# Kernel tuning notes

Measured on AMD Instinct MI355X. Metric: run time of the kernel, lower is better.

The kernel has to match this reference:

```python
import jax, jax.numpy as jnp
import numpy as np

N = 50000      # nodes
E = 800000     # edges (before self-loops)
F_IN = 256
H = 8          # heads layer 1
C = 64         # hidden channels per head
OUT = 40       # classes
NEG_SLOPE = 0.2


def setup_inputs() -> dict:
    key = jax.random.key(0)
    ks = jax.random.split(key, 10)
    sc = 0.05
    return {
        "x": jax.random.normal(ks[0], (N, F_IN), jnp.float32),
        "edge_index": jax.random.randint(ks[1], (2, E), 0, N, dtype=jnp.int64),
        "W1": jax.random.normal(ks[2], (F_IN, H * C), jnp.float32) * sc,
        "a_src1": jax.random.normal(ks[3], (H, C), jnp.float32) * sc,
        "a_dst1": jax.random.normal(ks[4], (H, C), jnp.float32) * sc,
        "b1": jnp.zeros((H * C,), jnp.float32),
        "W2": jax.random.normal(ks[5], (H * C, OUT), jnp.float32) * sc,
        "a_src2": jax.random.normal(ks[6], (1, OUT), jnp.float32) * sc,
        "a_dst2": jax.random.normal(ks[7], (1, OUT), jnp.float32) * sc,
        "b2": jnp.zeros((OUT,), jnp.float32),
    }


def gat_layer(h_in, src, dst, W, a_s, a_d, b, heads, ch, concat, n):
    # h: [n, heads, ch] per-head linear transform
    h = (h_in @ W).reshape(n, heads, ch)
    alpha_s = jnp.sum(h * a_s, axis=-1)   # [n, heads]
    alpha_d = jnp.sum(h * a_d, axis=-1)   # [n, heads]
    # edge-wise raw attention logits [E, heads]
    e = jax.nn.leaky_relu(alpha_s[src] + alpha_d[dst], NEG_SLOPE)
    # segment softmax over incoming edges of each dst node
    m = jax.ops.segment_max(e, dst, num_segments=n)
    w = jnp.exp(e - m[dst])
    s = jax.ops.segment_sum(w, dst, num_segments=n)
    alpha = w / s[dst]                    # [E, heads]
    # scatter-aggregate messages: [n, heads, ch]
    out = jax.ops.segment_sum(h[src] * alpha[:, :, None], dst, num_segments=n)
    out = out.reshape(n, heads * ch) if concat else out.mean(axis=1)
    return out + b


def reference(x, edge_index, W1, a_src1, a_dst1, b1, W2, a_src2, a_dst2, b2):
    # add self-loops (PyG GATConv default); guarantees every dst has >=1 edge
    loop = jnp.arange(N, dtype=edge_index.dtype)
    src = jnp.concatenate([edge_index[0], loop])
    dst = jnp.concatenate([edge_index[1], loop])
    h = gat_layer(x, src, dst, W1, a_src1, a_dst1, b1, H, C, True, N)
    h = jax.nn.relu(h)  # dropout is identity in eval mode
    out = gat_layer(h, src, dst, W2, a_src2, a_dst2, b2, 1, OUT, False, N)
    return jax.nn.log_softmax(out, axis=1)
```

## Files before the change

### kernel.cpp

```cpp
#include <hip/hip_runtime.h>

#define N_NODES 50000
#define N_EDGES 800000
#define F_INK   256
#define HC      512
#define OUT_C   40
#define OUT_P   48
#define NEG     0.2f
#define CAP     64
#define GEMM_NB 782
#define CHUNKS  782
#define PART_SZ 6250
#define SCAT_NB (CHUNKS * 8)

typedef short short8 __attribute__((ext_vector_type(8)));
typedef float f32x4 __attribute__((ext_vector_type(4)));
typedef float f32x2 __attribute__((ext_vector_type(2)));

__device__ __forceinline__ float bf2f(unsigned short u) {
    union { unsigned int i; float f; } v; v.i = ((unsigned int)u) << 16; return v.f;
}
__device__ __forceinline__ unsigned short f2bf(float f) {
    union { float f; unsigned int i; } v; v.f = f;
    unsigned int x = v.i;
    return (unsigned short)((x + 0x7fffu + ((x >> 16) & 1u)) >> 16);
}
__device__ __forceinline__ float bflo(unsigned int u) {
    union { unsigned int i; float f; } v; v.i = u << 16; return v.f;
}
__device__ __forceinline__ float bfhi(unsigned int u) {
    union { unsigned int i; float f; } v; v.i = u & 0xffff0000u; return v.f;
}
__device__ __forceinline__ bool ei_is64(const int* ei) {
    return ei[1] == 0 && ei[3] == 0 && ei[5] == 0;
}
__device__ __forceinline__ float lrelu(float x) { return fmaxf(x, NEG * x); }
__device__ __forceinline__ unsigned char f2fp8(float v) {
    return (unsigned char)(__builtin_amdgcn_cvt_pk_fp8_f32(v, v, 0, false) & 0xff);
}
__device__ __forceinline__ float fp82f(unsigned char b) {
    f32x2 p = __builtin_amdgcn_cvt_pk_f32_fp8((int)b, false);
    return p[0];
}

__global__ __launch_bounds__(256) void prep_k(const float* __restrict__ W1, const float* __restrict__ W2,
                       const float* __restrict__ s1, const float* __restrict__ d1, const float* __restrict__ b1,
                       const float* __restrict__ s2, const float* __restrict__ d2, const float* __restrict__ b2,
                       unsigned short* __restrict__ W1p, unsigned short* __restrict__ W2p,
                       unsigned short* __restrict__ s1c, unsigned short* __restrict__ d1c,
                       unsigned short* __restrict__ b1c, unsigned short* __restrict__ s2c,
                       unsigned short* __restrict__ d2c, unsigned short* __restrict__ b2c,
                       int* __restrict__ cnt) {
    int b = blockIdx.x;
    if (b < 512) {
        int t = b * 256 + threadIdx.x;
        int k = t / HC, n = t % HC;
        int s = k >> 5, q = (k >> 3) & 3, j = k & 7;
        W1p[((((s << 2) + q) * HC + n) << 3) + j] = f2bf(W1[k * HC + n]);
    } else if (b < 608) {
        int t = (b - 512) * 256 + threadIdx.x;
        int k = t / OUT_P, n = t % OUT_P;
        int s = k >> 5, q = (k >> 3) & 3, j = k & 7;
        unsigned short v = (n < OUT_C) ? f2bf(W2[k * OUT_C + n]) : (unsigned short)0;
        W2p[((((s << 2) + q) * OUT_P + n) << 3) + j] = v;
    } else if (b == 608) {
        int t = threadIdx.x;
        for (int j = t; j < 512; j += 256) {
            s1c[j] = f2bf(s1[j]); d1c[j] = f2bf(d1[j]); b1c[j] = f2bf(b1[j]);
        }
        if (t < OUT_C) { s2c[t] = f2bf(s2[t]); d2c[t] = f2bf(d2[t]); b2c[t] = f2bf(b2[t]); }
    } else {
        int i = (b - 609) * 256 + threadIdx.x;
        if (i < N_NODES) cnt[i * 16] = 0;
    }
}

__global__ __launch_bounds__(256) void scat_k(const int* __restrict__ ei,
                                              int* __restrict__ cnt, int* __restrict__ srcs) {
    int tid = threadIdx.x;
    int part = blockIdx.x & 7;
    int chunk = blockIdx.x >> 3;
    int lo = part * PART_SZ;
    bool is64 = ei_is64(ei);
    int e0 = chunk * 1024 + (tid << 2);
    int s[4], d[4];
    bool vld[4];
    if (chunk < CHUNKS - 1) {
        if (is64) {
            int4 a0 = *reinterpret_cast<const int4*>(ei + 2 * e0);
            int4 a1 = *reinterpret_cast<const int4*>(ei + 2 * e0 + 4);
            int4 c0 = *reinterpret_cast<const int4*>(ei + 2 * N_EDGES + 2 * e0);
            int4 c1 = *reinterpret_cast<const int4*>(ei + 2 * N_EDGES + 2 * e0 + 4);
            s[0] = a0.x; s[1] = a0.z; s[2] = a1.x; s[3] = a1.z;
            d[0] = c0.x; d[1] = c0.z; d[2] = c1.x; d[3] = c1.z;
        } else {
            int4 a0 = *reinterpret_cast<const int4*>(ei + e0);
            int4 c0 = *reinterpret_cast<const int4*>(ei + N_EDGES + e0);
            s[0] = a0.x; s[1] = a0.y; s[2] = a0.z; s[3] = a0.w;
            d[0] = c0.x; d[1] = c0.y; d[2] = c0.z; d[3] = c0.w;
        }
        vld[0] = vld[1] = vld[2] = vld[3] = true;
    } else {
#pragma unroll
        for (int j = 0; j < 4; j++) {
            int e = e0 + j;
            vld[j] = e < N_EDGES;
            int ec = vld[j] ? e : 0;
            s[j] = is64 ? ei[2 * ec] : ei[ec];
            d[j] = is64 ? ei[2 * N_EDGES + 2 * ec] : ei[N_EDGES + ec];
        }
    }
#pragma unroll
    for (int j = 0; j < 4; j++) {
        int dj = d[j];
        if (vld[j] && dj >= lo && dj < lo + PART_SZ) {
            int pos = atomicAdd(&cnt[dj * 16], 1);
            if (pos < CAP) srcs[(size_t)dj * CAP + pos] = s[j];
        }
    }
}

__global__ __launch_bounds__(256) void gemm1_k(const float* __restrict__ x,
                                               const unsigned short* __restrict__ Wp,
                                               const unsigned short* __restrict__ a_s,
                                               const unsigned short* __restrict__ a_d,
                                               unsigned char* __restrict__ h1f8,
                                               float* __restrict__ as1, float* __restrict__ ad1) {
    __shared__ unsigned short xs[64 * 264];
    int tid = threadIdx.x;
    int bm = blockIdx.x;
    int row0 = bm * 64;
#pragma unroll
    for (int it = 0; it < 16; it++) {
        int j = tid + it * 256;
        int r = j >> 6;
        int c = (j & 63) << 2;
        int rr = row0 + r; rr = rr < N_NODES ? rr : N_NODES - 1;
        float4 f = *reinterpret_cast<const float4*>(x + (size_t)rr * F_INK + c);
        unsigned int lo = (unsigned int)f2bf(f.x) | ((unsigned int)f2bf(f.y) << 16);
        unsigned int hi = (unsigned int)f2bf(f.z) | ((unsigned int)f2bf(f.w) << 16);
        *reinterpret_cast<uint2*>(&xs[r * 264 + c]) = make_uint2(lo, hi);
    }
    __syncthreads();
    int w = tid >> 6, lane = tid & 63;
    int q = lane >> 4, l16 = lane & 15;
    short8 a[8];
#pragma unroll
    for (int s = 0; s < 8; s++)
        a[s] = *reinterpret_cast<const short8*>(&xs[(w * 16 + l16) * 264 + s * 32 + q * 8]);
    int orow = row0 + w * 16 + q * 4;
#pragma unroll
    for (int bn = 0; bn < 8; bn++) {
        f32x4 acc[4];
#pragma unroll
        for (int t = 0; t < 4; t++) acc[t] = (f32x4){0.f, 0.f, 0.f, 0.f};
#pragma unroll
        for (int s = 0; s < 8; s++) {
#pragma unroll
            for (int t = 0; t < 4; t++) {
                int col = bn * 64 + t * 16 + l16;
                short8 b = *reinterpret_cast<const short8*>(Wp + ((((s << 2) + q) * HC + col) << 3));
                acc[t] = __builtin_amdgcn_mfma_f32_16x16x32_bf16(a[s], b, acc[t], 0, 0, 0);
            }
        }
        float sa0 = 0.f, sa1 = 0.f, sa2 = 0.f, sa3 = 0.f;
        float da0 = 0.f, da1 = 0.f, da2 = 0.f, da3 = 0.f;
#pragma unroll
        for (int t = 0; t < 4; t++) {
            int col = bn * 64 + t * 16 + l16;
            float asc = bf2f(a_s[col]);
            float adc = bf2f(a_d[col]);
            float v0 = acc[t][0], v1 = acc[t][1], v2 = acc[t][2], v3 = acc[t][3];
            sa0 += v0 * asc; da0 += v0 * adc;
            sa1 += v1 * asc; da1 += v1 * adc;
            sa2 += v2 * asc; da2 += v2 * adc;
            sa3 += v3 * asc; da3 += v3 * adc;
            if (orow + 3 < N_NODES) {
                h1f8[(size_t)(orow + 0) * HC + col] = f2fp8(v0);
                h1f8[(size_t)(orow + 1) * HC + col] = f2fp8(v1);
                h1f8[(size_t)(orow + 2) * HC + col] = f2fp8(v2);
                h1f8[(size_t)(orow + 3) * HC + col] = f2fp8(v3);
            } else {
                if (orow + 0 < N_NODES) h1f8[(size_t)(orow + 0) * HC + col] = f2fp8(v0);
                if (orow + 1 < N_NODES) h1f8[(size_t)(orow + 1) * HC + col] = f2fp8(v1);
                if (orow + 2 < N_NODES) h1f8[(size_t)(orow + 2) * HC + col] = f2fp8(v2);
                if (orow + 3 < N_NODES) h1f8[(size_t)(orow + 3) * HC + col] = f2fp8(v3);
            }
        }
#pragma unroll
        for (int m = 1; m < 16; m <<= 1) {
            sa0 += __shfl_xor(sa0, m, 64); sa1 += __shfl_xor(sa1, m, 64);
            sa2 += __shfl_xor(sa2, m, 64); sa3 += __shfl_xor(sa3, m, 64);
            da0 += __shfl_xor(da0, m, 64); da1 += __shfl_xor(da1, m, 64);
            da2 += __shfl_xor(da2, m, 64); da3 += __shfl_xor(da3, m, 64);
        }
        if (l16 < 4) {
            int rr = orow + l16;
            float sav = (l16 == 0) ? sa0 : (l16 == 1) ? sa1 : (l16 == 2) ? sa2 : sa3;
            float dav = (l16 == 0) ? da0 : (l16 == 1) ? da1 : (l16 == 2) ? da2 : da3;
            if (rr < N_NODES) { as1[rr * 8 + bn] = sav; ad1[rr * 8 + bn] = dav; }
        }
    }
}

#define ACC16(u, wgt)                                                              \
    {                                                                              \
        f32x2 q0 = __builtin_amdgcn_cvt_pk_f32_fp8((int)(u).x, false);             \
        f32x2 q1 = __builtin_amdgcn_cvt_pk_f32_fp8((int)(u).x, true);              \
        f32x2 q2 = __builtin_amdgcn_cvt_pk_f32_fp8((int)(u).y, false);             \
        f32x2 q3 = __builtin_amdgcn_cvt_pk_f32_fp8((int)(u).y, true);              \
        f32x2 q4 = __builtin_amdgcn_cvt_pk_f32_fp8((int)(u).z, false);             \
        f32x2 q5 = __builtin_amdgcn_cvt_pk_f32_fp8((int)(u).z, true);              \
        f32x2 q6 = __builtin_amdgcn_cvt_pk_f32_fp8((int)(u).w, false);             \
        f32x2 q7 = __builtin_amdgcn_cvt_pk_f32_fp8((int)(u).w, true);              \
        f32x2 wv = {(wgt), (wgt)};                                                 \
        ac[0] += wv * q0; ac[1] += wv * q1; ac[2] += wv * q2; ac[3] += wv * q3;    \
        ac[4] += wv * q4; ac[5] += wv * q5; ac[6] += wv * q6; ac[7] += wv * q7;    \
    }

__global__ __launch_bounds__(256) void agg1_k(const unsigned char* __restrict__ h1f8,
                                              const float* __restrict__ as1,
                                              const float* __restrict__ ad1,
                                              const int* __restrict__ cnt,
                                              const int* __restrict__ srcs,
                                              const unsigned short* __restrict__ b1,
                                              const unsigned short* __restrict__ W2p,
                                              const unsigned short* __restrict__ a_s2,
                                              const unsigned short* __restrict__ a_d2,
                                              unsigned char* __restrict__ h2f8) {
    __shared__ unsigned short rows[16 * 520];
    __shared__ int sSrc[16 * CAP];
    __shared__ int sCnt[16];
    __shared__ float sAs[16], sAd[16];
    __shared__ int ctr;
    int tid = threadIdx.x;
    int base = blockIdx.x * 16;
    reinterpret_cast<int4*>(sSrc)[tid] =
        reinterpret_cast<const int4*>(srcs + (size_t)base * CAP)[tid];
    if (tid < 16) {
        int d = cnt[(base + tid) * 16];
        sCnt[tid] = d < CAP ? d : CAP;
        sAs[tid] = 0.f; sAd[tid] = 0.f;
    }
    if (tid == 0) ctr = 0;
    __syncthreads();
    int w = tid >> 6, lane = tid & 63;
    int half = lane >> 5, li = lane & 31;
    int h = li >> 2;
    uint4 ub0 = reinterpret_cast<const uint4*>(b1)[li * 2 + 0];
    uint4 ub1 = reinterpret_cast<const uint4*>(b1)[li * 2 + 1];
    for (;;) {
        int rl = 0;
        if (lane == 0) rl = atomicAdd(&ctr, 1);
        rl = __shfl(rl, 0, 64);
        if (rl >= 16) break;
        int wid = base + rl;
        float adv = ad1[wid * 8 + h];
        const int* sp = sSrc + rl * CAP;
        int deg = sCnt[rl];
        f32x2 ac[8];
#pragma unroll
        for (int k = 0; k < 8; k++) ac[k] = (f32x2){0.f, 0.f};
        float sumw = 0.f;
        {
            int s = half ? (deg > 0 ? sp[0] : wid) : wid;
            float A = as1[s * 8 + h];
            uint4 u = reinterpret_cast<const uint4*>(h1f8 + (size_t)s * HC)[li];
            float wj = (half && deg == 0) ? 0.f : __expf(lrelu(A + adv));
            sumw += wj;
            ACC16(u, wj)
        }
        int v = 1;
        for (; v + 16 <= deg; v += 16) {
            int s[8]; float A[8]; uint4 u[8];
#pragma unroll
            for (int j = 0; j < 8; j++) s[j] = sp[v + 2 * j + half];
#pragma unroll
            for (int j = 0; j < 8; j++) A[j] = as1[s[j] * 8 + h];
#pragma unroll
            for (int j = 0; j < 8; j++)
                u[j] = reinterpret_cast<const uint4*>(h1f8 + (size_t)s[j] * HC)[li];
#pragma unroll
            for (int j = 0; j < 8; j++) {
                float wj = __expf(lrelu(A[j] + adv));
                sumw += wj;
                ACC16(u[j], wj)
            }
        }
        for (; v + 8 <= deg; v += 8) {
            int s[4]; float A[4]; uint4 u[4];
#pragma unroll
            for (int j = 0; j < 4; j++) s[j] = sp[v + 2 * j + half];
#pragma unroll
            for (int j = 0; j < 4; j++) A[j] = as1[s[j] * 8 + h];
#pragma unroll
            for (int j = 0; j < 4; j++)
                u[j] = reinterpret_cast<const uint4*>(h1f8 + (size_t)s[j] * HC)[li];
#pragma unroll
            for (int j = 0; j < 4; j++) {
                float wj = __expf(lrelu(A[j] + adv));
                sumw += wj;
                ACC16(u[j], wj)
            }
        }
        for (; v + 4 <= deg; v += 4) {
            int s[2]; float A[2]; uint4 u[2];
#pragma unroll
            for (int j = 0; j < 2; j++) s[j] = sp[v + 2 * j + half];
#pragma unroll
            for (int j = 0; j < 2; j++) A[j] = as1[s[j] * 8 + h];
#pragma unroll
            for (int j = 0; j < 2; j++)
                u[j] = reinterpret_cast<const uint4*>(h1f8 + (size_t)s[j] * HC)[li];
#pragma unroll
            for (int j = 0; j < 2; j++) {
                float wj = __expf(lrelu(A[j] + adv));
                sumw += wj;
                ACC16(u[j], wj)
            }
        }
        for (; v < deg; v += 2) {
            int vv = v + half;
            bool ok = vv < deg;
            int s = ok ? sp[vv] : wid;
            float A = as1[s * 8 + h];
            uint4 u = reinterpret_cast<const uint4*>(h1f8 + (size_t)s * HC)[li];
            float wj = ok ? __expf(lrelu(A + adv)) : 0.f;
            sumw += wj;
            ACC16(u, wj)
        }
        sumw += __shfl_xor(sumw, 32, 64);
#pragma unroll
        for (int k = 0; k < 8; k++) {
            ac[k][0] += __shfl_xor(ac[k][0], 32, 64);
            ac[k][1] += __shfl_xor(ac[k][1], 32, 64);
        }
        float inv = 1.f / sumw;
        f32x2 n0 = half ? ac[4] : ac[0];
        f32x2 n1 = half ? ac[5] : ac[1];
        f32x2 n2 = half ? ac[6] : ac[2];
        f32x2 n3 = half ? ac[7] : ac[3];
        uint4 ubh = half ? ub1 : ub0;
        float o0 = fmaxf(n0[0] * inv + bflo(ubh.x), 0.f);
        float o1 = fmaxf(n0[1] * inv + bfhi(ubh.x), 0.f);
        float o2 = fmaxf(n1[0] * inv + bflo(ubh.y), 0.f);
        float o3 = fmaxf(n1[1] * inv + bfhi(ubh.y), 0.f);
        float o4 = fmaxf(n2[0] * inv + bflo(ubh.z), 0.f);
        float o5 = fmaxf(n2[1] * inv + bfhi(ubh.z), 0.f);
        float o6 = fmaxf(n3[0] * inv + bflo(ubh.w), 0.f);
        float o7 = fmaxf(n3[1] * inv + bfhi(ubh.w), 0.f);
        uint4 r;
        r.x = (unsigned int)f2bf(o0) | ((unsigned int)f2bf(o1) << 16);
        r.y = (unsigned int)f2bf(o2) | ((unsigned int)f2bf(o3) << 16);
        r.z = (unsigned int)f2bf(o4) | ((unsigned int)f2bf(o5) << 16);
        r.w = (unsigned int)f2bf(o6) | ((unsigned int)f2bf(o7) << 16);
        *reinterpret_cast<uint4*>(&rows[rl * 520 + li * 16 + half * 8]) = r;
    }
    __syncthreads();
    if (w < 3) {
        int q = lane >> 4, l16 = lane & 15;
        int col = w * 16 + l16;
        f32x4 acc = (f32x4){0.f, 0.f, 0.f, 0.f};
#pragma unroll
        for (int s = 0; s < HC / 32; s++) {
            short8 a = *reinterpret_cast<const short8*>(&rows[l16 * 520 + s * 32 + q * 8]);
            short8 b = *reinterpret_cast<const short8*>(W2p + ((((s << 2) + q) * OUT_P + col) << 3));
            acc = __builtin_amdgcn_mfma_f32_16x16x32_bf16(a, b, acc, 0, 0, 0);
        }
        float sa0 = 0.f, sa1 = 0.f, sa2 = 0.f, sa3 = 0.f;
        float da0 = 0.f, da1 = 0.f, da2 = 0.f, da3 = 0.f;
        if (col < OUT_C) {
            float asc = bf2f(a_s2[col]);
            float adc = bf2f(a_d2[col]);
            sa0 = acc[0] * asc; da0 = acc[0] * adc;
            sa1 = acc[1] * asc; da1 = acc[1] * adc;
            sa2 = acc[2] * asc; da2 = acc[2] * adc;
            sa3 = acc[3] * asc; da3 = acc[3] * adc;
#pragma unroll
            for (int r = 0; r < 4; r++)
                h2f8[(size_t)(base + q * 4 + r) * 64 + col] = f2fp8(acc[r]);
        }
#pragma unroll
        for (int m = 1; m < 16; m <<= 1) {
            sa0 += __shfl_xor(sa0, m, 64); sa1 += __shfl_xor(sa1, m, 64);
            sa2 += __shfl_xor(sa2, m, 64); sa3 += __shfl_xor(sa3, m, 64);
            da0 += __shfl_xor(da0, m, 64); da1 += __shfl_xor(da1, m, 64);
            da2 += __shfl_xor(da2, m, 64); da3 += __shfl_xor(da3, m, 64);
        }
        if (l16 < 4) {
            int rr = q * 4 + l16;
            float sav = (l16 == 0) ? sa0 : (l16 == 1) ? sa1 : (l16 == 2) ? sa2 : sa3;
            float dav = (l16 == 0) ? da0 : (l16 == 1) ? da1 : (l16 == 2) ? da2 : da3;
            atomicAdd(&sAs[rr], sav);
            atomicAdd(&sAd[rr], dav);
        }
    }
    __syncthreads();
    if (tid < 16) {
        unsigned char* r = h2f8 + (size_t)(base + tid) * 64;
        *reinterpret_cast<float*>(r + 40) = sAs[tid];
        *reinterpret_cast<float*>(r + 44) = sAd[tid];
    }
}

__global__ __launch_bounds__(256) void agg2_k(const unsigned char* __restrict__ h2f8,
                                              const int* __restrict__ cnt,
                                              const int* __restrict__ srcs,
                                              const unsigned short* __restrict__ b2,
                                              float* __restrict__ outp) {
    __shared__ int sSrc[4 * CAP];
    __shared__ int sCnt[4];
    int tid = threadIdx.x;
    int base = blockIdx.x * 4;
    if (tid < 64)
        reinterpret_cast<int4*>(sSrc)[tid] =
            reinterpret_cast<const int4*>(srcs + (size_t)base * CAP)[tid];
    if (tid < 4) {
        int d = cnt[(base + tid) * 16];
        sCnt[tid] = d < CAP ? d : CAP;
    }
    __syncthreads();
    int w = tid >> 6;
    int wid = base + w;
    int lane = tid & 63;
    bool act = lane < OUT_C;
    int lclamp = act ? lane : 0;
    const unsigned char* rd = h2f8 + (size_t)wid * 64;
    float adv = *reinterpret_cast<const float*>(rd + 44);
    float acc, sumw;
    {
        float w0 = __expf(lrelu(*reinterpret_cast<const float*>(rd + 40) + adv));
        sumw = w0;
        acc = w0 * fp82f(rd[lclamp]);
    }
    const int* sp = sSrc + w * CAP;
    int deg = sCnt[w];
    int v = 0;
    for (; v + 8 <= deg; v += 8) {
        const unsigned char* r[8];
        float A[8];
        unsigned char c[8];
#pragma unroll
        for (int j = 0; j < 8; j++) r[j] = h2f8 + (size_t)sp[v + j] * 64;
#pragma unroll
        for (int j = 0; j < 8; j++) A[j] = *reinterpret_cast<const float*>(r[j] + 40);
#pragma unroll
        for (int j = 0; j < 8; j++) c[j] = r[j][lclamp];
#pragma unroll
        for (int j = 0; j < 8; j++) {
            float wj = __expf(lrelu(A[j] + adv));
            sumw += wj;
            acc += wj * fp82f(c[j]);
        }
    }
    for (; v + 4 <= deg; v += 4) {
        const unsigned char* r[4];
        float A[4];
        unsigned char c[4];
#pragma unroll
        for (int j = 0; j < 4; j++) r[j] = h2f8 + (size_t)sp[v + j] * 64;
#pragma unroll
        for (int j = 0; j < 4; j++) A[j] = *reinterpret_cast<const float*>(r[j] + 40);
#pragma unroll
        for (int j = 0; j < 4; j++) c[j] = r[j][lclamp];
#pragma unroll
        for (int j = 0; j < 4; j++) {
            float wj = __expf(lrelu(A[j] + adv));
            sumw += wj;
            acc += wj * fp82f(c[j]);
        }
    }
    for (; v < deg; v++) {
        const unsigned char* r0 = h2f8 + (size_t)sp[v] * 64;
        float w0 = __expf(lrelu(*reinterpret_cast<const float*>(r0 + 40) + adv));
        sumw += w0;
        acc += w0 * fp82f(r0[lclamp]);
    }
    float o = acc / sumw + bf2f(b2[lclamp]);
    float mval = act ? o : -1e30f;
#pragma unroll
    for (int m = 32; m >= 1; m >>= 1) mval = fmaxf(mval, __shfl_xor(mval, m, 64));
    float ex = act ? __expf(o - mval) : 0.f;
#pragma unroll
    for (int m = 32; m >= 1; m >>= 1) ex += __shfl_xor(ex, m, 64);
    float res = o - mval - __logf(ex);
    if (act) outp[(size_t)wid * OUT_C + lane] = res;
}

extern "C" void kernel_launch(void* const* d_in, const int* in_sizes, int n_in,
                              void* d_out, int out_size, void* d_ws, size_t ws_size,
                              hipStream_t stream) {
    const float* x      = (const float*)d_in[0];
    const int*   ei     = (const int*)d_in[1];
    const float* W1     = (const float*)d_in[2];
    const float* as1raw = (const float*)d_in[3];
    const float* ad1raw = (const float*)d_in[4];
    const float* b1raw  = (const float*)d_in[5];
    const float* W2     = (const float*)d_in[6];
    const float* as2raw = (const float*)d_in[7];
    const float* ad2raw = (const float*)d_in[8];
    const float* b2raw  = (const float*)d_in[9];
    float* out = (float*)d_out;

    char* p = (char*)d_ws;
    auto alloc = [&](size_t bytes) -> char* {
        char* r = p;
        p += (bytes + 255) & ~(size_t)255;
        return r;
    };
    unsigned short* s1c  = (unsigned short*)alloc(512 * 2);
    unsigned short* d1c  = (unsigned short*)alloc(512 * 2);
    unsigned short* b1c  = (unsigned short*)alloc(512 * 2);
    unsigned short* s2c  = (unsigned short*)alloc(OUT_C * 2);
    unsigned short* d2c  = (unsigned short*)alloc(OUT_C * 2);
    unsigned short* b2c  = (unsigned short*)alloc(OUT_C * 2);
    unsigned char*  h1f8 = (unsigned char*)alloc((size_t)N_NODES * HC);
    unsigned char*  h2f8 = (unsigned char*)alloc((size_t)N_NODES * 64);
    float* as1  = (float*)alloc((size_t)N_NODES * 8 * 4);
    float* ad1  = (float*)alloc((size_t)N_NODES * 8 * 4);
    int* cnt    = (int*)alloc((size_t)N_NODES * 64);
    int* srcs   = (int*)alloc((size_t)N_NODES * CAP * 4);
    unsigned short* W1p = (unsigned short*)alloc((size_t)F_INK * HC * 2);
    unsigned short* W2p = (unsigned short*)alloc((size_t)HC * OUT_P * 2);
    (void)ws_size; (void)in_sizes; (void)n_in; (void)out_size;

    const int NB = (N_NODES + 255) / 256;

    prep_k<<<609 + NB, 256, 0, stream>>>(W1, W2, as1raw, ad1raw, b1raw, as2raw, ad2raw, b2raw,
                                         W1p, W2p, s1c, d1c, b1c, s2c, d2c, b2c, cnt);
    gemm1_k<<<GEMM_NB, 256, 0, stream>>>(x, W1p, s1c, d1c, h1f8, as1, ad1);
    scat_k<<<SCAT_NB, 256, 0, stream>>>(ei, cnt, srcs);
    agg1_k<<<N_NODES / 16, 256, 0, stream>>>(h1f8, as1, ad1, cnt, srcs, b1c,
                                             W2p, s2c, d2c, h2f8);
    agg2_k<<<N_NODES / 4, 256, 0, stream>>>(h2f8, cnt, srcs, b2c, out);
}
```

Baseline: 290.2 us.

## Split layer-1 aggregation per head, add separate gemm2, merge scatter into gemm1

The edge-scatter kernel is folded into the gemm1 launch as extra blocks, so bucketing edges by destination can run alongside the first GEMM. The fused layer-1 aggregation plus layer-2 GEMM kernel is split in two. The new aggregation kernel gives each (16-node group, head) pair its own block, with 16-lane groups gathering 4 fp8 bytes per edge. It writes bf16 hidden rows to a new global buffer, which a separate gemm2 kernel reloads for the MFMA projection. This raises parallelism and cuts per-block register pressure. The cost is a round trip of roughly 51 MB through global memory and narrower, less coalesced per-head gathers.

```diff
diff --git a/kernel.cpp b/kernel.cpp
--- a/kernel.cpp
+++ b/kernel.cpp
@@ -16,6 +16,8 @@
 typedef short short8 __attribute__((ext_vector_type(8)));
 typedef float f32x4 __attribute__((ext_vector_type(4)));
 typedef float f32x2 __attribute__((ext_vector_type(2)));
+typedef int   iv4  __attribute__((ext_vector_type(4)));
+typedef unsigned int uv2 __attribute__((ext_vector_type(2)));
 
 __device__ __forceinline__ float bf2f(unsigned short u) {
     union { unsigned int i; float f; } v; v.i = ((unsigned int)u) << 16; return v.f;
@@ -75,59 +77,60 @@
     }
 }
 
-__global__ __launch_bounds__(256) void scat_k(const int* __restrict__ ei,
-                                              int* __restrict__ cnt, int* __restrict__ srcs) {
-    int tid = threadIdx.x;
-    int part = blockIdx.x & 7;
-    int chunk = blockIdx.x >> 3;
-    int lo = part * PART_SZ;
-    bool is64 = ei_is64(ei);
-    int e0 = chunk * 1024 + (tid << 2);
-    int s[4], d[4];
-    bool vld[4];
-    if (chunk < CHUNKS - 1) {
-        if (is64) {
-            int4 a0 = *reinterpret_cast<const int4*>(ei + 2 * e0);
-            int4 a1 = *reinterpret_cast<const int4*>(ei + 2 * e0 + 4);
-            int4 c0 = *reinterpret_cast<const int4*>(ei + 2 * N_EDGES + 2 * e0);
-            int4 c1 = *reinterpret_cast<const int4*>(ei + 2 * N_EDGES + 2 * e0 + 4);
-            s[0] = a0.x; s[1] = a0.z; s[2] = a1.x; s[3] = a1.z;
-            d[0] = c0.x; d[1] = c0.z; d[2] = c1.x; d[3] = c1.z;
-        } else {
-            int4 a0 = *reinterpret_cast<const int4*>(ei + e0);
-            int4 c0 = *reinterpret_cast<const int4*>(ei + N_EDGES + e0);
-            s[0] = a0.x; s[1] = a0.y; s[2] = a0.z; s[3] = a0.w;
-            d[0] = c0.x; d[1] = c0.y; d[2] = c0.z; d[3] = c0.w;
-        }
-        vld[0] = vld[1] = vld[2] = vld[3] = true;
-    } else {
-#pragma unroll
-        for (int j = 0; j < 4; j++) {
-            int e = e0 + j;
-            vld[j] = e < N_EDGES;
-            int ec = vld[j] ? e : 0;
-            s[j] = is64 ? ei[2 * ec] : ei[ec];
-            d[j] = is64 ? ei[2 * N_EDGES + 2 * ec] : ei[N_EDGES + ec];
-        }
-    }
-#pragma unroll
-    for (int j = 0; j < 4; j++) {
-        int dj = d[j];
-        if (vld[j] && dj >= lo && dj < lo + PART_SZ) {
-            int pos = atomicAdd(&cnt[dj * 16], 1);
-            if (pos < CAP) srcs[(size_t)dj * CAP + pos] = s[j];
-        }
-    }
-}
-
 __global__ __launch_bounds__(256) void gemm1_k(const float* __restrict__ x,
                                                const unsigned short* __restrict__ Wp,
                                                const unsigned short* __restrict__ a_s,
                                                const unsigned short* __restrict__ a_d,
                                                unsigned char* __restrict__ h1f8,
-                                               float* __restrict__ as1, float* __restrict__ ad1) {
+                                               float* __restrict__ as1, float* __restrict__ ad1,
+                                               const int* __restrict__ ei,
+                                               int* __restrict__ cnt, int* __restrict__ srcs) {
     __shared__ unsigned short xs[64 * 264];
     int tid = threadIdx.x;
+    if (blockIdx.x >= GEMM_NB) {
+        int sb = blockIdx.x - GEMM_NB;
+        int part = blockIdx.x & 7;
+        int chunk = sb >> 3;
+        int lo = part * PART_SZ;
+        bool is64 = ei_is64(ei);
+        int e0 = chunk * 1024 + (tid << 2);
+        int s[4], d[4];
+        bool vld[4];
+        if (chunk < CHUNKS - 1) {
+            if (is64) {
+                int4 a0 = *reinterpret_cast<const int4*>(ei + 2 * e0);
+                int4 a1 = *reinterpret_cast<const int4*>(ei + 2 * e0 + 4);
+                int4 c0 = *reinterpret_cast<const int4*>(ei + 2 * N_EDGES + 2 * e0);
+                int4 c1 = *reinterpret_cast<const int4*>(ei + 2 * N_EDGES + 2 * e0 + 4);
+                s[0] = a0.x; s[1] = a0.z; s[2] = a1.x; s[3] = a1.z;
+                d[0] = c0.x; d[1] = c0.z; d[2] = c1.x; d[3] = c1.z;
+            } else {
+                int4 a0 = *reinterpret_cast<const int4*>(ei + e0);
+                int4 c0 = *reinterpret_cast<const int4*>(ei + N_EDGES + e0);
+                s[0] = a0.x; s[1] = a0.y; s[2] = a0.z; s[3] = a0.w;
+                d[0] = c0.x; d[1] = c0.y; d[2] = c0.z; d[3] = c0.w;
+            }
+            vld[0] = vld[1] = vld[2] = vld[3] = true;
+        } else {
+#pragma unroll
+            for (int j = 0; j < 4; j++) {
+                int e = e0 + j;
+                vld[j] = e < N_EDGES;
+                int ec = vld[j] ? e : 0;
+                s[j] = is64 ? ei[2 * ec] : ei[ec];
+                d[j] = is64 ? ei[2 * N_EDGES + 2 * ec] : ei[N_EDGES + ec];
+            }
+        }
+#pragma unroll
+        for (int j = 0; j < 4; j++) {
+            int dj = d[j];
+            if (vld[j] && dj >= lo && dj < lo + PART_SZ) {
+                int pos = atomicAdd(&cnt[dj * 16], 1);
+                if (pos < CAP) srcs[(size_t)dj * CAP + pos] = s[j];
+            }
+        }
+        return;
+    }
     int bm = blockIdx.x;
     int row0 = bm * 64;
 #pragma unroll
@@ -203,52 +206,35 @@
     }
 }
 
-#define ACC16(u, wgt)                                                              \
-    {                                                                              \
-        f32x2 q0 = __builtin_amdgcn_cvt_pk_f32_fp8((int)(u).x, false);             \
-        f32x2 q1 = __builtin_amdgcn_cvt_pk_f32_fp8((int)(u).x, true);              \
-        f32x2 q2 = __builtin_amdgcn_cvt_pk_f32_fp8((int)(u).y, false);             \
-        f32x2 q3 = __builtin_amdgcn_cvt_pk_f32_fp8((int)(u).y, true);              \
-        f32x2 q4 = __builtin_amdgcn_cvt_pk_f32_fp8((int)(u).z, false);             \
-        f32x2 q5 = __builtin_amdgcn_cvt_pk_f32_fp8((int)(u).z, true);              \
-        f32x2 q6 = __builtin_amdgcn_cvt_pk_f32_fp8((int)(u).w, false);             \
-        f32x2 q7 = __builtin_amdgcn_cvt_pk_f32_fp8((int)(u).w, true);              \
-        f32x2 wv = {(wgt), (wgt)};                                                 \
-        ac[0] += wv * q0; ac[1] += wv * q1; ac[2] += wv * q2; ac[3] += wv * q3;    \
-        ac[4] += wv * q4; ac[5] += wv * q5; ac[6] += wv * q6; ac[7] += wv * q7;    \
-    }
-
-__global__ __launch_bounds__(256) void agg1_k(const unsigned char* __restrict__ h1f8,
-                                              const float* __restrict__ as1,
-                                              const float* __restrict__ ad1,
-                                              const int* __restrict__ cnt,
-                                              const int* __restrict__ srcs,
-                                              const unsigned short* __restrict__ b1,
-                                              const unsigned short* __restrict__ W2p,
-                                              const unsigned short* __restrict__ a_s2,
-                                              const unsigned short* __restrict__ a_d2,
-                                              unsigned char* __restrict__ h2f8) {
-    __shared__ unsigned short rows[16 * 520];
+__global__ __launch_bounds__(256) void agg1h_k(const unsigned char* __restrict__ h1f8,
+                                               const float* __restrict__ as1,
+                                               const float* __restrict__ ad1,
+                                               const int* __restrict__ cnt,
+                                               const int* __restrict__ srcs,
+                                               const unsigned short* __restrict__ b1,
+                                               unsigned short* __restrict__ rows_g) {
     __shared__ int sSrc[16 * CAP];
     __shared__ int sCnt[16];
-    __shared__ float sAs[16], sAd[16];
     __shared__ int ctr;
     int tid = threadIdx.x;
-    int base = blockIdx.x * 16;
-    reinterpret_cast<int4*>(sSrc)[tid] =
-        reinterpret_cast<const int4*>(srcs + (size_t)base * CAP)[tid];
+    int h = blockIdx.x & 7;
+    int base = (blockIdx.x >> 3) * 16;
     if (tid < 16) {
         int d = cnt[(base + tid) * 16];
         sCnt[tid] = d < CAP ? d : CAP;
-        sAs[tid] = 0.f; sAd[tid] = 0.f;
     }
     if (tid == 0) ctr = 0;
     __syncthreads();
-    int w = tid >> 6, lane = tid & 63;
-    int half = lane >> 5, li = lane & 31;
-    int h = li >> 2;
-    uint4 ub0 = reinterpret_cast<const uint4*>(b1)[li * 2 + 0];
-    uint4 ub1 = reinterpret_cast<const uint4*>(b1)[li * 2 + 1];
+    {
+        int row = tid >> 4, col = tid & 15;
+        if (col * 4 < sCnt[row])
+            reinterpret_cast<iv4*>(sSrc)[tid] = __builtin_nontemporal_load(
+                reinterpret_cast<const iv4*>(srcs + (size_t)base * CAP) + tid);
+    }
+    __syncthreads();
+    int lane = tid & 63;
+    int g = lane & 15, q = lane >> 4;
+    uint2 ubb = *reinterpret_cast<const uint2*>(b1 + h * 64 + g * 4);
     for (;;) {
         int rl = 0;
         if (lane == 0) rl = atomicAdd(&ctr, 1);
@@ -257,106 +243,91 @@
         int wid = base + rl;
         float adv = ad1[wid * 8 + h];
         const int* sp = sSrc + rl * CAP;
-        int deg = sCnt[rl];
-        f32x2 ac[8];
-#pragma unroll
-        for (int k = 0; k < 8; k++) ac[k] = (f32x2){0.f, 0.f};
+        int n = sCnt[rl] + 1;
+        f32x2 a01 = {0.f, 0.f}, a23 = {0.f, 0.f};
         float sumw = 0.f;
-        {
-            int s = half ? (deg > 0 ? sp[0] : wid) : wid;
-            float A = as1[s * 8 + h];
-            uint4 u = reinterpret_cast<const uint4*>(h1f8 + (size_t)s * HC)[li];
-            float wj = (half && deg == 0) ? 0.f : __expf(lrelu(A + adv));
-            sumw += wj;
-            ACC16(u, wj)
-        }
-        int v = 1;
-        for (; v + 16 <= deg; v += 16) {
-            int s[8]; float A[8]; uint4 u[8];
-#pragma unroll
-            for (int j = 0; j < 8; j++) s[j] = sp[v + 2 * j + half];
-#pragma unroll
-            for (int j = 0; j < 8; j++) A[j] = as1[s[j] * 8 + h];
-#pragma unroll
-            for (int j = 0; j < 8; j++)
-                u[j] = reinterpret_cast<const uint4*>(h1f8 + (size_t)s[j] * HC)[li];
-#pragma unroll
-            for (int j = 0; j < 8; j++) {
-                float wj = __expf(lrelu(A[j] + adv));
+        int v = 0;
+        for (; v + 16 <= n; v += 16) {
+            int s_[4]; float A_[4]; unsigned int u_[4];
+#pragma unroll
+            for (int j = 0; j < 4; j++) {
+                int idx = v + 4 * j + q;
+                s_[j] = (idx == 0) ? wid : sp[idx - 1];
+            }
+#pragma unroll
+            for (int j = 0; j < 4; j++) A_[j] = as1[s_[j] * 8 + h];
+#pragma unroll
+            for (int j = 0; j < 4; j++)
+                u_[j] = *reinterpret_cast<const unsigned int*>(
+                    h1f8 + (size_t)s_[j] * HC + h * 64 + (g << 2));
+#pragma unroll
+            for (int j = 0; j < 4; j++) {
+                float wj = __expf(lrelu(A_[j] + adv));
                 sumw += wj;
-                ACC16(u[j], wj)
-            }
-        }
-        for (; v + 8 <= deg; v += 8) {
-            int s[4]; float A[4]; uint4 u[4];
-#pragma unroll
-            for (int j = 0; j < 4; j++) s[j] = sp[v + 2 * j + half];
-#pragma unroll
-            for (int j = 0; j < 4; j++) A[j] = as1[s[j] * 8 + h];
-#pragma unroll
-            for (int j = 0; j < 4; j++)
-                u[j] = reinterpret_cast<const uint4*>(h1f8 + (size_t)s[j] * HC)[li];
-#pragma unroll
-            for (int j = 0; j < 4; j++) {
-                float wj = __expf(lrelu(A[j] + adv));
-                sumw += wj;
-                ACC16(u[j], wj)
-            }
-        }
-        for (; v + 4 <= deg; v += 4) {
-            int s[2]; float A[2]; uint4 u[2];
-#pragma unroll
-            for (int j = 0; j < 2; j++) s[j] = sp[v + 2 * j + half];
-#pragma unroll
-            for (int j = 0; j < 2; j++) A[j] = as1[s[j] * 8 + h];
-#pragma unroll
-            for (int j = 0; j < 2; j++)
-                u[j] = reinterpret_cast<const uint4*>(h1f8 + (size_t)s[j] * HC)[li];
-#pragma unroll
-            for (int j = 0; j < 2; j++) {
-                float wj = __expf(lrelu(A[j] + adv));
-                sumw += wj;
-                ACC16(u[j], wj)
-            }
-        }
-        for (; v < deg; v += 2) {
-            int vv = v + half;
-            bool ok = vv < deg;
-            int s = ok ? sp[vv] : wid;
-            float A = as1[s * 8 + h];
-            uint4 u = reinterpret_cast<const uint4*>(h1f8 + (size_t)s * HC)[li];
+                f32x2 wv = {wj, wj};
+                f32x2 p0 = __builtin_amdgcn_cvt_pk_f32_fp8((int)u_[j], false);
+                f32x2 p1 = __builtin_amdgcn_cvt_pk_f32_fp8((int)u_[j], true);
+                a01 += wv * p0; a23 += wv * p1;
+            }
+        }
+        for (; v < n; v += 4) {
+            int idx = v + q;
+            bool ok = idx < n;
+            int ic = ok ? idx : 0;
+            int s0 = (ic == 0) ? wid : sp[ic - 1];
+            float A = as1[s0 * 8 + h];
+            unsigned int u = *reinterpret_cast<const unsigned int*>(
+                h1f8 + (size_t)s0 * HC + h * 64 + (g << 2));
             float wj = ok ? __expf(lrelu(A + adv)) : 0.f;
             sumw += wj;
-            ACC16(u, wj)
-        }
-        sumw += __shfl_xor(sumw, 32, 64);
-#pragma unroll
-        for (int k = 0; k < 8; k++) {
-            ac[k][0] += __shfl_xor(ac[k][0], 32, 64);
-            ac[k][1] += __shfl_xor(ac[k][1], 32, 64);
-        }
-        float inv = 1.f / sumw;
-        f32x2 n0 = half ? ac[4] : ac[0];
-        f32x2 n1 = half ? ac[5] : ac[1];
-        f32x2 n2 = half ? ac[6] : ac[2];
-        f32x2 n3 = half ? ac[7] : ac[3];
-        uint4 ubh = half ? ub1 : ub0;
-        float o0 = fmaxf(n0[0] * inv + bflo(ubh.x), 0.f);
-        float o1 = fmaxf(n0[1] * inv + bfhi(ubh.x), 0.f);
-        float o2 = fmaxf(n1[0] * inv + bflo(ubh.y), 0.f);
-        float o3 = fmaxf(n1[1] * inv + bfhi(ubh.y), 0.f);
-        float o4 = fmaxf(n2[0] * inv + bflo(ubh.z), 0.f);
-        float o5 = fmaxf(n2[1] * inv + bfhi(ubh.z), 0.f);
-        float o6 = fmaxf(n3[0] * inv + bflo(ubh.w), 0.f);
-        float o7 = fmaxf(n3[1] * inv + bfhi(ubh.w), 0.f);
-        uint4 r;
-        r.x = (unsigned int)f2bf(o0) | ((unsigned int)f2bf(o1) << 16);
-        r.y = (unsigned int)f2bf(o2) | ((unsigned int)f2bf(o3) << 16);
-        r.z = (unsigned int)f2bf(o4) | ((unsigned int)f2bf(o5) << 16);
-        r.w = (unsigned int)f2bf(o6) | ((unsigned int)f2bf(o7) << 16);
-        *reinterpret_cast<uint4*>(&rows[rl * 520 + li * 16 + half * 8]) = r;
+            f32x2 wv = {wj, wj};
+            f32x2 p0 = __builtin_amdgcn_cvt_pk_f32_fp8((int)u, false);
+            f32x2 p1 = __builtin_amdgcn_cvt_pk_f32_fp8((int)u, true);
+            a01 += wv * p0; a23 += wv * p1;
+        }
+#pragma unroll
+        for (int m = 16; m <= 32; m <<= 1) {
+            sumw += __shfl_xor(sumw, m, 64);
+            a01[0] += __shfl_xor(a01[0], m, 64);
+            a01[1] += __shfl_xor(a01[1], m, 64);
+            a23[0] += __shfl_xor(a23[0], m, 64);
+            a23[1] += __shfl_xor(a23[1], m, 64);
+        }
+        if (lane < 16) {
+            float inv = 1.f / sumw;
+            float o0 = fmaxf(a01[0] * inv + bflo(ubb.x), 0.f);
+            float o1 = fmaxf(a01[1] * inv + bfhi(ubb.x), 0.f);
+            float o2 = fmaxf(a23[0] * inv + bflo(ubb.y), 0.f);
+            float o3 = fmaxf(a23[1] * inv + bfhi(ubb.y), 0.f);
+            uv2 r;
+            r.x = (unsigned int)f2bf(o0) | ((unsigned int)f2bf(o1) << 16);
+            r.y = (unsigned int)f2bf(o2) | ((unsigned int)f2bf(o3) << 16);
+            __builtin_nontemporal_store(r, reinterpret_cast<uv2*>(
+                rows_g + (size_t)wid * HC + h * 64 + lane * 4));
+        }
+    }
+}
+
+__global__ __launch_bounds__(256) void gemm2_k(const unsigned short* __restrict__ rows_g,
+                                               const unsigned short* __restrict__ W2p,
+                                               const unsigned short* __restrict__ a_s2,
+                                               const unsigned short* __restrict__ a_d2,
+                                               unsigned char* __restrict__ h2f8) {
+    __shared__ unsigned short rows[16 * 520];
+    __shared__ float sAs[16], sAd[16];
+    int tid = threadIdx.x;
+    int base = blockIdx.x * 16;
+    if (tid < 16) { sAs[tid] = 0.f; sAd[tid] = 0.f; }
+    {
+        int r = tid >> 4, seg = tid & 15;
+        const uint4* gp = reinterpret_cast<const uint4*>(
+            rows_g + (size_t)(base + r) * HC + seg * 32);
+        uint4* lp = reinterpret_cast<uint4*>(&rows[r * 520 + seg * 32]);
+#pragma unroll
+        for (int j = 0; j < 4; j++) lp[j] = gp[j];
     }
     __syncthreads();
+    int w = tid >> 6, lane = tid & 63;
     if (w < 3) {
         int q = lane >> 4, l16 = lane & 15;
         int col = w * 16 + l16;
@@ -516,6 +487,7 @@
     unsigned short* b2c  = (unsigned short*)alloc(OUT_C * 2);
     unsigned char*  h1f8 = (unsigned char*)alloc((size_t)N_NODES * HC);
     unsigned char*  h2f8 = (unsigned char*)alloc((size_t)N_NODES * 64);
+    unsigned short* rows = (unsigned short*)alloc((size_t)N_NODES * HC * 2);
     float* as1  = (float*)alloc((size_t)N_NODES * 8 * 4);
     float* ad1  = (float*)alloc((size_t)N_NODES * 8 * 4);
     int* cnt    = (int*)alloc((size_t)N_NODES * 64);
@@ -528,9 +500,9 @@
 
     prep_k<<<609 + NB, 256, 0, stream>>>(W1, W2, as1raw, ad1raw, b1raw, as2raw, ad2raw, b2raw,
                                          W1p, W2p, s1c, d1c, b1c, s2c, d2c, b2c, cnt);
-    gemm1_k<<<GEMM_NB, 256, 0, stream>>>(x, W1p, s1c, d1c, h1f8, as1, ad1);
-    scat_k<<<SCAT_NB, 256, 0, stream>>>(ei, cnt, srcs);
-    agg1_k<<<N_NODES / 16, 256, 0, stream>>>(h1f8, as1, ad1, cnt, srcs, b1c,
-                                             W2p, s2c, d2c, h2f8);
+    gemm1_k<<<GEMM_NB + SCAT_NB, 256, 0, stream>>>(x, W1p, s1c, d1c, h1f8, as1, ad1,
+                                                   ei, cnt, srcs);
+    agg1h_k<<<(N_NODES / 16) * 8, 256, 0, stream>>>(h1f8, as1, ad1, cnt, srcs, b1c, rows);
+    gemm2_k<<<N_NODES / 16, 256, 0, stream>>>(rows, W2p, s2c, d2c, h2f8);
     agg2_k<<<N_NODES / 4, 256, 0, stream>>>(h2f8, cnt, srcs, b2c, out);
 }
```

Result: slower. 359.3 us (+23.8%).

## Fuse edge scatter into GEMM launch and double agg1 block to 32 nodes

Applied to the files above, without the earlier changes.

The edge-scatter kernel becomes extra blocks of the first GEMM launch, so bucketing edges by destination can overlap with the dense transform and one launch is dropped. The first aggregation kernel now uses 512-thread blocks covering 32 destination nodes, with two wave groups each running the layer-2 MFMA projection on 16 rows. Bounds checks handle the partial last block. Larger blocks use more LDS per block, which may reduce occupancy.

```diff
diff --git a/kernel.cpp b/kernel.cpp
--- a/kernel.cpp
+++ b/kernel.cpp
@@ -75,59 +75,60 @@
     }
 }
 
-__global__ __launch_bounds__(256) void scat_k(const int* __restrict__ ei,
-                                              int* __restrict__ cnt, int* __restrict__ srcs) {
-    int tid = threadIdx.x;
-    int part = blockIdx.x & 7;
-    int chunk = blockIdx.x >> 3;
-    int lo = part * PART_SZ;
-    bool is64 = ei_is64(ei);
-    int e0 = chunk * 1024 + (tid << 2);
-    int s[4], d[4];
-    bool vld[4];
-    if (chunk < CHUNKS - 1) {
-        if (is64) {
-            int4 a0 = *reinterpret_cast<const int4*>(ei + 2 * e0);
-            int4 a1 = *reinterpret_cast<const int4*>(ei + 2 * e0 + 4);
-            int4 c0 = *reinterpret_cast<const int4*>(ei + 2 * N_EDGES + 2 * e0);
-            int4 c1 = *reinterpret_cast<const int4*>(ei + 2 * N_EDGES + 2 * e0 + 4);
-            s[0] = a0.x; s[1] = a0.z; s[2] = a1.x; s[3] = a1.z;
-            d[0] = c0.x; d[1] = c0.z; d[2] = c1.x; d[3] = c1.z;
-        } else {
-            int4 a0 = *reinterpret_cast<const int4*>(ei + e0);
-            int4 c0 = *reinterpret_cast<const int4*>(ei + N_EDGES + e0);
-            s[0] = a0.x; s[1] = a0.y; s[2] = a0.z; s[3] = a0.w;
-            d[0] = c0.x; d[1] = c0.y; d[2] = c0.z; d[3] = c0.w;
-        }
-        vld[0] = vld[1] = vld[2] = vld[3] = true;
-    } else {
-#pragma unroll
-        for (int j = 0; j < 4; j++) {
-            int e = e0 + j;
-            vld[j] = e < N_EDGES;
-            int ec = vld[j] ? e : 0;
-            s[j] = is64 ? ei[2 * ec] : ei[ec];
-            d[j] = is64 ? ei[2 * N_EDGES + 2 * ec] : ei[N_EDGES + ec];
-        }
-    }
-#pragma unroll
-    for (int j = 0; j < 4; j++) {
-        int dj = d[j];
-        if (vld[j] && dj >= lo && dj < lo + PART_SZ) {
-            int pos = atomicAdd(&cnt[dj * 16], 1);
-            if (pos < CAP) srcs[(size_t)dj * CAP + pos] = s[j];
-        }
-    }
-}
-
 __global__ __launch_bounds__(256) void gemm1_k(const float* __restrict__ x,
                                                const unsigned short* __restrict__ Wp,
                                                const unsigned short* __restrict__ a_s,
                                                const unsigned short* __restrict__ a_d,
                                                unsigned char* __restrict__ h1f8,
-                                               float* __restrict__ as1, float* __restrict__ ad1) {
+                                               float* __restrict__ as1, float* __restrict__ ad1,
+                                               const int* __restrict__ ei,
+                                               int* __restrict__ cnt, int* __restrict__ srcs) {
     __shared__ unsigned short xs[64 * 264];
     int tid = threadIdx.x;
+    if (blockIdx.x >= GEMM_NB) {
+        int sb = blockIdx.x - GEMM_NB;
+        int part = blockIdx.x & 7;
+        int chunk = sb >> 3;
+        int lo = part * PART_SZ;
+        bool is64 = ei_is64(ei);
+        int e0 = chunk * 1024 + (tid << 2);
+        int s[4], d[4];
+        bool vld[4];
+        if (chunk < CHUNKS - 1) {
+            if (is64) {
+                int4 a0 = *reinterpret_cast<const int4*>(ei + 2 * e0);
+                int4 a1 = *reinterpret_cast<const int4*>(ei + 2 * e0 + 4);
+                int4 c0 = *reinterpret_cast<const int4*>(ei + 2 * N_EDGES + 2 * e0);
+                int4 c1 = *reinterpret_cast<const int4*>(ei + 2 * N_EDGES + 2 * e0 + 4);
+                s[0] = a0.x; s[1] = a0.z; s[2] = a1.x; s[3] = a1.z;
+                d[0] = c0.x; d[1] = c0.z; d[2] = c1.x; d[3] = c1.z;
+            } else {
+                int4 a0 = *reinterpret_cast<const int4*>(ei + e0);
+                int4 c0 = *reinterpret_cast<const int4*>(ei + N_EDGES + e0);
+                s[0] = a0.x; s[1] = a0.y; s[2] = a0.z; s[3] = a0.w;
+                d[0] = c0.x; d[1] = c0.y; d[2] = c0.z; d[3] = c0.w;
+            }
+            vld[0] = vld[1] = vld[2] = vld[3] = true;
+        } else {
+#pragma unroll
+            for (int j = 0; j < 4; j++) {
+                int e = e0 + j;
+                vld[j] = e < N_EDGES;
+                int ec = vld[j] ? e : 0;
+                s[j] = is64 ? ei[2 * ec] : ei[ec];
+                d[j] = is64 ? ei[2 * N_EDGES + 2 * ec] : ei[N_EDGES + ec];
+            }
+        }
+#pragma unroll
+        for (int j = 0; j < 4; j++) {
+            int dj = d[j];
+            if (vld[j] && dj >= lo && dj < lo + PART_SZ) {
+                int pos = atomicAdd(&cnt[dj * 16], 1);
+                if (pos < CAP) srcs[(size_t)dj * CAP + pos] = s[j];
+            }
+        }
+        return;
+    }
     int bm = blockIdx.x;
     int row0 = bm * 64;
 #pragma unroll
@@ -218,7 +219,7 @@
         ac[4] += wv * q4; ac[5] += wv * q5; ac[6] += wv * q6; ac[7] += wv * q7;    \
     }
 
-__global__ __launch_bounds__(256) void agg1_k(const unsigned char* __restrict__ h1f8,
+__global__ __launch_bounds__(512) void agg1_k(const unsigned char* __restrict__ h1f8,
                                               const float* __restrict__ as1,
                                               const float* __restrict__ ad1,
                                               const int* __restrict__ cnt,
@@ -228,23 +229,27 @@
                                               const unsigned short* __restrict__ a_s2,
                                               const unsigned short* __restrict__ a_d2,
                                               unsigned char* __restrict__ h2f8) {
-    __shared__ unsigned short rows[16 * 520];
-    __shared__ int sSrc[16 * CAP];
-    __shared__ int sCnt[16];
-    __shared__ float sAs[16], sAd[16];
+    __shared__ unsigned short rows[32 * 520];
+    __shared__ int sSrc[32 * CAP];
+    __shared__ int sCnt[32];
+    __shared__ float sAs[32], sAd[32];
     __shared__ int ctr;
     int tid = threadIdx.x;
-    int base = blockIdx.x * 16;
-    reinterpret_cast<int4*>(sSrc)[tid] =
-        reinterpret_cast<const int4*>(srcs + (size_t)base * CAP)[tid];
-    if (tid < 16) {
-        int d = cnt[(base + tid) * 16];
-        sCnt[tid] = d < CAP ? d : CAP;
+    int base = blockIdx.x * 32;
+    int nd = N_NODES - base; nd = nd < 32 ? nd : 32;
+    if ((tid >> 4) < nd)
+        reinterpret_cast<int4*>(sSrc)[tid] =
+            reinterpret_cast<const int4*>(srcs + (size_t)base * CAP)[tid];
+    if (tid < 32) {
         sAs[tid] = 0.f; sAd[tid] = 0.f;
+        if (tid < nd) {
+            int d = cnt[(base + tid) * 16];
+            sCnt[tid] = d < CAP ? d : CAP;
+        } else sCnt[tid] = 0;
     }
     if (tid == 0) ctr = 0;
     __syncthreads();
-    int w = tid >> 6, lane = tid & 63;
+    int lane = tid & 63;
     int half = lane >> 5, li = lane & 31;
     int h = li >> 2;
     uint4 ub0 = reinterpret_cast<const uint4*>(b1)[li * 2 + 0];
@@ -253,7 +258,7 @@
         int rl = 0;
         if (lane == 0) rl = atomicAdd(&ctr, 1);
         rl = __shfl(rl, 0, 64);
-        if (rl >= 16) break;
+        if (rl >= nd) break;
         int wid = base + rl;
         float adv = ad1[wid * 8 + h];
         const int* sp = sSrc + rl * CAP;
@@ -357,13 +362,16 @@
         *reinterpret_cast<uint4*>(&rows[rl * 520 + li * 16 + half * 8]) = r;
     }
     __syncthreads();
-    if (w < 3) {
+    int w = tid >> 6;
+    int grp = w >> 2, wl = w & 3;
+    if (wl < 3) {
+        int rbase = grp * 16;
         int q = lane >> 4, l16 = lane & 15;
-        int col = w * 16 + l16;
+        int col = wl * 16 + l16;
         f32x4 acc = (f32x4){0.f, 0.f, 0.f, 0.f};
 #pragma unroll
         for (int s = 0; s < HC / 32; s++) {
-            short8 a = *reinterpret_cast<const short8*>(&rows[l16 * 520 + s * 32 + q * 8]);
+            short8 a = *reinterpret_cast<const short8*>(&rows[(rbase + l16) * 520 + s * 32 + q * 8]);
             short8 b = *reinterpret_cast<const short8*>(W2p + ((((s << 2) + q) * OUT_P + col) << 3));
             acc = __builtin_amdgcn_mfma_f32_16x16x32_bf16(a, b, acc, 0, 0, 0);
         }
@@ -377,8 +385,11 @@
             sa2 = acc[2] * asc; da2 = acc[2] * adc;
             sa3 = acc[3] * asc; da3 = acc[3] * adc;
 #pragma unroll
-            for (int r = 0; r < 4; r++)
-                h2f8[(size_t)(base + q * 4 + r) * 64 + col] = f2fp8(acc[r]);
+            for (int r = 0; r < 4; r++) {
+                int node = base + rbase + q * 4 + r;
+                if (node < N_NODES)
+                    h2f8[(size_t)node * 64 + col] = f2fp8(acc[r]);
+            }
         }
 #pragma unroll
         for (int m = 1; m < 16; m <<= 1) {
@@ -388,7 +399,7 @@
             da2 += __shfl_xor(da2, m, 64); da3 += __shfl_xor(da3, m, 64);
         }
         if (l16 < 4) {
-            int rr = q * 4 + l16;
+            int rr = rbase + q * 4 + l16;
             float sav = (l16 == 0) ? sa0 : (l16 == 1) ? sa1 : (l16 == 2) ? sa2 : sa3;
             float dav = (l16 == 0) ? da0 : (l16 == 1) ? da1 : (l16 == 2) ? da2 : da3;
             atomicAdd(&sAs[rr], sav);
@@ -396,7 +407,7 @@
         }
     }
     __syncthreads();
-    if (tid < 16) {
+    if (tid < 32 && base + tid < N_NODES) {
         unsigned char* r = h2f8 + (size_t)(base + tid) * 64;
         *reinterpret_cast<float*>(r + 40) = sAs[tid];
         *reinterpret_cast<float*>(r + 44) = sAd[tid];
@@ -528,9 +539,9 @@
 
     prep_k<<<609 + NB, 256, 0, stream>>>(W1, W2, as1raw, ad1raw, b1raw, as2raw, ad2raw, b2raw,
                                          W1p, W2p, s1c, d1c, b1c, s2c, d2c, b2c, cnt);
-    gemm1_k<<<GEMM_NB, 256, 0, stream>>>(x, W1p, s1c, d1c, h1f8, as1, ad1);
-    scat_k<<<SCAT_NB, 256, 0, stream>>>(ei, cnt, srcs);
-    agg1_k<<<N_NODES / 16, 256, 0, stream>>>(h1f8, as1, ad1, cnt, srcs, b1c,
-                                             W2p, s2c, d2c, h2f8);
+    gemm1_k<<<GEMM_NB + SCAT_NB, 256, 0, stream>>>(x, W1p, s1c, d1c, h1f8, as1, ad1,
+                                                   ei, cnt, srcs);
+    agg1_k<<<(N_NODES + 31) / 32, 512, 0, stream>>>(h1f8, as1, ad1, cnt, srcs, b1c,
+                                                    W2p, s2c, d2c, h2f8);
     agg2_k<<<N_NODES / 4, 256, 0, stream>>>(h2f8, cnt, srcs, b2c, out);
 }
```

Result: faster. 272.5 us (-6.1%).

## Fuse edge scatter into GEMM1 launch with XCC-affine partition claiming

Applied to the files above, without the earlier changes.

Folds the edge-scatter kernel into the gemm1 launch as extra blocks, so the two independent stages overlap on the GPU and one launch is removed. Each scatter block reads its XCC ID and atomically claims a destination partition, starting from the one matching its XCC, so that atomics on a given partition's counters tend to come from the same die's L2. A claim array is added and zeroed in the prep kernel. This costs an extra atomic handshake per block and makes GEMM and scatter compete for the same CUs.

```diff
diff --git a/kernel.cpp b/kernel.cpp
--- a/kernel.cpp
+++ b/kernel.cpp
@@ -50,7 +50,7 @@
                        unsigned short* __restrict__ s1c, unsigned short* __restrict__ d1c,
                        unsigned short* __restrict__ b1c, unsigned short* __restrict__ s2c,
                        unsigned short* __restrict__ d2c, unsigned short* __restrict__ b2c,
-                       int* __restrict__ cnt) {
+                       int* __restrict__ cnt, int* __restrict__ claim) {
     int b = blockIdx.x;
     if (b < 512) {
         int t = b * 256 + threadIdx.x;
@@ -69,54 +69,12 @@
             s1c[j] = f2bf(s1[j]); d1c[j] = f2bf(d1[j]); b1c[j] = f2bf(b1[j]);
         }
         if (t < OUT_C) { s2c[t] = f2bf(s2[t]); d2c[t] = f2bf(d2[t]); b2c[t] = f2bf(b2[t]); }
-    } else {
+    } else if (b < 805) {
         int i = (b - 609) * 256 + threadIdx.x;
         if (i < N_NODES) cnt[i * 16] = 0;
-    }
-}
-
-__global__ __launch_bounds__(256) void scat_k(const int* __restrict__ ei,
-                                              int* __restrict__ cnt, int* __restrict__ srcs) {
-    int tid = threadIdx.x;
-    int part = blockIdx.x & 7;
-    int chunk = blockIdx.x >> 3;
-    int lo = part * PART_SZ;
-    bool is64 = ei_is64(ei);
-    int e0 = chunk * 1024 + (tid << 2);
-    int s[4], d[4];
-    bool vld[4];
-    if (chunk < CHUNKS - 1) {
-        if (is64) {
-            int4 a0 = *reinterpret_cast<const int4*>(ei + 2 * e0);
-            int4 a1 = *reinterpret_cast<const int4*>(ei + 2 * e0 + 4);
-            int4 c0 = *reinterpret_cast<const int4*>(ei + 2 * N_EDGES + 2 * e0);
-            int4 c1 = *reinterpret_cast<const int4*>(ei + 2 * N_EDGES + 2 * e0 + 4);
-            s[0] = a0.x; s[1] = a0.z; s[2] = a1.x; s[3] = a1.z;
-            d[0] = c0.x; d[1] = c0.z; d[2] = c1.x; d[3] = c1.z;
-        } else {
-            int4 a0 = *reinterpret_cast<const int4*>(ei + e0);
-            int4 c0 = *reinterpret_cast<const int4*>(ei + N_EDGES + e0);
-            s[0] = a0.x; s[1] = a0.y; s[2] = a0.z; s[3] = a0.w;
-            d[0] = c0.x; d[1] = c0.y; d[2] = c0.z; d[3] = c0.w;
-        }
-        vld[0] = vld[1] = vld[2] = vld[3] = true;
     } else {
-#pragma unroll
-        for (int j = 0; j < 4; j++) {
-            int e = e0 + j;
-            vld[j] = e < N_EDGES;
-            int ec = vld[j] ? e : 0;
-            s[j] = is64 ? ei[2 * ec] : ei[ec];
-            d[j] = is64 ? ei[2 * N_EDGES + 2 * ec] : ei[N_EDGES + ec];
-        }
-    }
-#pragma unroll
-    for (int j = 0; j < 4; j++) {
-        int dj = d[j];
-        if (vld[j] && dj >= lo && dj < lo + PART_SZ) {
-            int pos = atomicAdd(&cnt[dj * 16], 1);
-            if (pos < CAP) srcs[(size_t)dj * CAP + pos] = s[j];
-        }
+        int i = (b - 805) * 256 + threadIdx.x;
+        if (i < CHUNKS * 8) claim[i] = 0;
     }
 }
 
@@ -125,9 +83,71 @@
                                                const unsigned short* __restrict__ a_s,
                                                const unsigned short* __restrict__ a_d,
                                                unsigned char* __restrict__ h1f8,
-                                               float* __restrict__ as1, float* __restrict__ ad1) {
+                                               float* __restrict__ as1, float* __restrict__ ad1,
+                                               const int* __restrict__ ei,
+                                               int* __restrict__ cnt, int* __restrict__ srcs,
+                                               int* __restrict__ claim) {
     __shared__ unsigned short xs[64 * 264];
     int tid = threadIdx.x;
+    if (blockIdx.x >= GEMM_NB) {
+        __shared__ int sPart;
+        int sb = blockIdx.x - GEMM_NB;
+        int chunk = sb >> 3;
+        if (tid == 0) {
+            unsigned int xcc;
+            asm volatile("s_getreg_b32 %0, hwreg(HW_REG_XCC_ID)" : "=s"(xcc));
+            int pref = (int)(xcc & 7u);
+            int got = 0;
+#pragma unroll
+            for (int t = 0; t < 8; t++) {
+                int cand = (pref + t) & 7;
+                if (!got && atomicExch(&claim[chunk * 8 + cand], 1) == 0) {
+                    sPart = cand; got = 1;
+                }
+            }
+        }
+        __syncthreads();
+        int part = sPart;
+        int lo = part * PART_SZ;
+        bool is64 = ei_is64(ei);
+        int e0 = chunk * 1024 + (tid << 2);
+        int s[4], d[4];
+        bool vld[4];
+        if (chunk < CHUNKS - 1) {
+            if (is64) {
+                int4 a0 = *reinterpret_cast<const int4*>(ei + 2 * e0);
+                int4 a1 = *reinterpret_cast<const int4*>(ei + 2 * e0 + 4);
+                int4 c0 = *reinterpret_cast<const int4*>(ei + 2 * N_EDGES + 2 * e0);
+                int4 c1 = *reinterpret_cast<const int4*>(ei + 2 * N_EDGES + 2 * e0 + 4);
+                s[0] = a0.x; s[1] = a0.z; s[2] = a1.x; s[3] = a1.z;
+                d[0] = c0.x; d[1] = c0.z; d[2] = c1.x; d[3] = c1.z;
+            } else {
+                int4 a0 = *reinterpret_cast<const int4*>(ei + e0);
+                int4 c0 = *reinterpret_cast<const int4*>(ei + N_EDGES + e0);
+                s[0] = a0.x; s[1] = a0.y; s[2] = a0.z; s[3] = a0.w;
+                d[0] = c0.x; d[1] = c0.y; d[2] = c0.z; d[3] = c0.w;
+            }
+            vld[0] = vld[1] = vld[2] = vld[3] = true;
+        } else {
+#pragma unroll
+            for (int j = 0; j < 4; j++) {
+                int e = e0 + j;
+                vld[j] = e < N_EDGES;
+                int ec = vld[j] ? e : 0;
+                s[j] = is64 ? ei[2 * ec] : ei[ec];
+                d[j] = is64 ? ei[2 * N_EDGES + 2 * ec] : ei[N_EDGES + ec];
+            }
+        }
+#pragma unroll
+        for (int j = 0; j < 4; j++) {
+            int dj = d[j];
+            if (vld[j] && dj >= lo && dj < lo + PART_SZ) {
+                int pos = atomicAdd(&cnt[dj * 16], 1);
+                if (pos < CAP) srcs[(size_t)dj * CAP + pos] = s[j];
+            }
+        }
+        return;
+    }
     int bm = blockIdx.x;
     int row0 = bm * 64;
 #pragma unroll
@@ -520,16 +540,18 @@
     float* ad1  = (float*)alloc((size_t)N_NODES * 8 * 4);
     int* cnt    = (int*)alloc((size_t)N_NODES * 64);
     int* srcs   = (int*)alloc((size_t)N_NODES * CAP * 4);
+    int* claim  = (int*)alloc((size_t)CHUNKS * 8 * 4);
     unsigned short* W1p = (unsigned short*)alloc((size_t)F_INK * HC * 2);
     unsigned short* W2p = (unsigned short*)alloc((size_t)HC * OUT_P * 2);
     (void)ws_size; (void)in_sizes; (void)n_in; (void)out_size;
 
     const int NB = (N_NODES + 255) / 256;
-
-    prep_k<<<609 + NB, 256, 0, stream>>>(W1, W2, as1raw, ad1raw, b1raw, as2raw, ad2raw, b2raw,
-                                         W1p, W2p, s1c, d1c, b1c, s2c, d2c, b2c, cnt);
-    gemm1_k<<<GEMM_NB, 256, 0, stream>>>(x, W1p, s1c, d1c, h1f8, as1, ad1);
-    scat_k<<<SCAT_NB, 256, 0, stream>>>(ei, cnt, srcs);
+    const int CB = (CHUNKS * 8 + 255) / 256;
+
+    prep_k<<<609 + NB + CB, 256, 0, stream>>>(W1, W2, as1raw, ad1raw, b1raw, as2raw, ad2raw, b2raw,
+                                              W1p, W2p, s1c, d1c, b1c, s2c, d2c, b2c, cnt, claim);
+    gemm1_k<<<GEMM_NB + SCAT_NB, 256, 0, stream>>>(x, W1p, s1c, d1c, h1f8, as1, ad1,
+                                                   ei, cnt, srcs, claim);
     agg1_k<<<N_NODES / 16, 256, 0, stream>>>(h1f8, as1, ad1, cnt, srcs, b1c,
                                              W2p, s2c, d2c, h2f8);
     agg2_k<<<N_NODES / 4, 256, 0, stream>>>(h2f8, cnt, srcs, b2c, out);
```

Measured after the change: 269.8 us. 7.0% less time.
